# Kernel tuning notes

Hardware: AMD Instinct MI355X
Metric: run time of the kernel (lower is better)

## Reference

```python
import jax, jax.numpy as jnp
import numpy as np

B, T, D = 64, 196, 768
H = 12          # num_heads
HID = 64        # lstm hidden dim per direction


def setup_inputs() -> dict:
    key = jax.random.key(0)
    ks = jax.random.split(key, 13)
    s = 0.02
    return {
        "x": jax.random.normal(ks[0], (B, T, D), jnp.float32),
        "pre_W": jax.random.normal(ks[1], (D, D), jnp.float32) * s,
        "pre_b": jax.random.normal(ks[2], (D,), jnp.float32) * s,
        "Wih_f": jax.random.normal(ks[3], (H, 4 * HID, D // H), jnp.float32) * s,
        "Whh_f": jax.random.normal(ks[4], (H, 4 * HID, HID), jnp.float32) * s,
        "bih_f": jax.random.normal(ks[5], (H, 4 * HID), jnp.float32) * s,
        "bhh_f": jax.random.normal(ks[6], (H, 4 * HID), jnp.float32) * s,
        "Wih_r": jax.random.normal(ks[7], (H, 4 * HID, D // H), jnp.float32) * s,
        "Whh_r": jax.random.normal(ks[8], (H, 4 * HID, HID), jnp.float32) * s,
        "bih_r": jax.random.normal(ks[9], (H, 4 * HID), jnp.float32) * s,
        "bhh_r": jax.random.normal(ks[10], (H, 4 * HID), jnp.float32) * s,
        "proj_W": jax.random.normal(ks[11], (D, 2 * H * HID), jnp.float32) * s,
        "proj_b": jax.random.normal(ks[12], (D,), jnp.float32) * s,
    }


def _lstm_dir(xh, Wih, Whh, bih, bhh):
    """xh: [H, B, T, d]; weights stacked over heads. Returns [H, B, T, HID].
    Gate order i, f, g, o (PyTorch convention)."""
    hid = Whh.shape[-1]

    def one_head(xc, wih, whh, bi, bh):
        # precompute input contribution for all timesteps: [B, T, 4*hid]
        gx = jnp.einsum('btd,gd->btg', xc, wih) + bi + bh

        def step(carry, g_t):
            h, c = carry
            g = g_t + h @ whh.T
            i, f, gg, o = jnp.split(g, 4, axis=-1)
            i = jax.nn.sigmoid(i)
            f = jax.nn.sigmoid(f)
            gg = jnp.tanh(gg)
            o = jax.nn.sigmoid(o)
            c = f * c + i * gg
            h = o * jnp.tanh(c)
            return (h, c), h

        b = xc.shape[0]
        h0 = jnp.zeros((b, hid), xc.dtype)
        _, hs = jax.lax.scan(step, (h0, h0), gx.transpose(1, 0, 2))  # [T, B, hid]
        return hs.transpose(1, 0, 2)  # [B, T, hid]

    return jax.vmap(one_head)(xh, Wih, Whh, bih, bhh)


def reference(x, pre_W, pre_b, Wih_f, Whh_f, bih_f, bhh_f,
              Wih_r, Whh_r, bih_r, bhh_r, proj_W, proj_b):
    x = x @ pre_W.T + pre_b                      # pre_proj
    b, t, dm = x.shape
    h = Wih_f.shape[0]
    d = dm // h
    xh = x.reshape(b, t, h, d).transpose(2, 0, 1, 3)   # [H, B, T, d] (chunk along last dim)

    y_f = _lstm_dir(xh, Wih_f, Whh_f, bih_f, bhh_f)               # [H, B, T, hid]
    y_r = _lstm_dir(xh[:, :, ::-1], Wih_r, Whh_r, bih_r, bhh_r)[:, :, ::-1]

    hid = y_f.shape[-1]
    # concat fwd outputs of all heads, then rev outputs of all heads
    yf = y_f.transpose(1, 2, 0, 3).reshape(b, t, h * hid)
    yr = y_r.transpose(1, 2, 0, 3).reshape(b, t, h * hid)
    y_cat = jnp.concatenate([yf, yr], axis=-1)   # [B, T, 2*H*hid]
    return y_cat @ proj_W.T + proj_b
```

## Files before the change

kernel.cpp:

```cpp
#include <hip/hip_runtime.h>
#include <hip/hip_bf16.h>
#include <cstdint>
#include <cstddef>

#define B_   64
#define T_   196
#define D_   768
#define H_   12
#define HID_ 64
#define NT_  (B_ * T_)

typedef __attribute__((ext_vector_type(8))) __bf16 bf16x8;
typedef __attribute__((ext_vector_type(4))) float  f32x4;

__device__ __forceinline__ float bf2f(uint16_t u) {
    uint32_t x = ((uint32_t)u) << 16;
    return __builtin_bit_cast(float, x);
}
__device__ __forceinline__ uint16_t f2bf(float f) {
    uint32_t x = __builtin_bit_cast(uint32_t, f);
    uint32_t r = (x + 0x7fffu + ((x >> 16) & 1u)) >> 16;
    return (uint16_t)r;
}
__device__ __forceinline__ __bf16 f2bfv(float f) {
    return __builtin_bit_cast(__bf16, f2bf(f));
}

__device__ __forceinline__ float sigm(float x) {
    return __builtin_amdgcn_rcpf(1.f + __expf(-x));
}
__device__ __forceinline__ float tanh_f(float x) {
    return 1.f - 2.f * __builtin_amdgcn_rcpf(1.f + __expf(2.f * x));
}

__device__ __forceinline__ int swzg(int row, int col) {
    int b = (row << 6) + (col << 1);
    b ^= (row & 7) << 4;
    return b >> 1;
}
__device__ __forceinline__ int swzA(int row, int col) {
    int b = (row << 8) + (col << 1);
    b ^= (row & 7) << 4;
    return b >> 1;
}

__global__ __launch_bounds__(256)
void f32_to_bf16_k(const float* __restrict__ in, uint16_t* __restrict__ out, int n4)
{
    int i = blockIdx.x * 256 + threadIdx.x;
    const int stride = gridDim.x * 256;
    for (; i < n4; i += stride) {
        float4 v = ((const float4*)in)[i];
        ushort4 o;
        o.x = f2bf(v.x); o.y = f2bf(v.y); o.z = f2bf(v.z); o.w = f2bf(v.w);
        ((ushort4*)out)[i] = o;
    }
}

template<int KDIM, bool A_F32, bool OUT_BF16>
__global__ __launch_bounds__(256) __attribute__((amdgpu_waves_per_eu(2)))
void gemm_nt_mfma(const void* __restrict__ Aab, const uint16_t* __restrict__ Bw,
                  const float* __restrict__ bias, void* __restrict__ Cout, int Mtot)
{
    constexpr int NK = KDIM / 32;
    __shared__ uint16_t smA[2][128 * 32];
    __shared__ uint16_t smB[2][128 * 32];

    const int tid = threadIdx.x, lane = tid & 63, wv = tid >> 6;
    const int n0 = blockIdx.x * 128, m0 = blockIdx.y * 128;
    const int wr = wv >> 1, wc = wv & 1;
    const int fr = lane & 15;
    const int fk8 = (lane >> 4) * 8;

    const int srow = tid >> 1;
    const int scol = (tid & 1) * 16;

    const float*    Af = (const float*)Aab;
    const uint16_t* Ab = (const uint16_t*)Aab;

    f32x4 acc[4][4];
#pragma unroll
    for (int i = 0; i < 4; ++i)
#pragma unroll
        for (int j = 0; j < 4; ++j) acc[i][j] = (f32x4){0.f, 0.f, 0.f, 0.f};

    uint4 rA0, rA1, rB0, rB1;

    auto loadA = [&](int k0) {
        if constexpr (A_F32) {
            const float* p = Af + (size_t)(n0 + srow) * KDIM + k0 + scol;
            float4 a0 = *(const float4*)(p);
            float4 a1 = *(const float4*)(p + 4);
            float4 a2 = *(const float4*)(p + 8);
            float4 a3 = *(const float4*)(p + 12);
            rA0.x = (uint32_t)f2bf(a0.x) | ((uint32_t)f2bf(a0.y) << 16);
            rA0.y = (uint32_t)f2bf(a0.z) | ((uint32_t)f2bf(a0.w) << 16);
            rA0.z = (uint32_t)f2bf(a1.x) | ((uint32_t)f2bf(a1.y) << 16);
            rA0.w = (uint32_t)f2bf(a1.z) | ((uint32_t)f2bf(a1.w) << 16);
            rA1.x = (uint32_t)f2bf(a2.x) | ((uint32_t)f2bf(a2.y) << 16);
            rA1.y = (uint32_t)f2bf(a2.z) | ((uint32_t)f2bf(a2.w) << 16);
            rA1.z = (uint32_t)f2bf(a3.x) | ((uint32_t)f2bf(a3.y) << 16);
            rA1.w = (uint32_t)f2bf(a3.z) | ((uint32_t)f2bf(a3.w) << 16);
        } else {
            const uint16_t* p = Ab + (size_t)(n0 + srow) * KDIM + k0 + scol;
            rA0 = *(const uint4*)p;
            rA1 = *(const uint4*)(p + 8);
        }
    };
    auto loadB = [&](int k0) {
        const uint16_t* p = Bw + (size_t)(m0 + srow) * KDIM + k0 + scol;
        rB0 = *(const uint4*)p;
        rB1 = *(const uint4*)(p + 8);
    };
    auto dsWrite = [&](int buf) {
        *(uint4*)&smA[buf][swzg(srow, scol)]     = rA0;
        *(uint4*)&smA[buf][swzg(srow, scol + 8)] = rA1;
        *(uint4*)&smB[buf][swzg(srow, scol)]     = rB0;
        *(uint4*)&smB[buf][swzg(srow, scol + 8)] = rB1;
    };

    loadA(0); loadB(0);
    dsWrite(0);

    for (int kt = 0; kt < NK; ++kt) {
        __syncthreads();
        const int buf = kt & 1;
        const bool more = (kt + 1) < NK;
        if (more) { loadA(32 * (kt + 1)); loadB(32 * (kt + 1)); }

        bf16x8 af[4], bfg[4];
#pragma unroll
        for (int i = 0; i < 4; ++i)
            af[i] = *(const bf16x8*)&smA[buf][swzg(64 * wr + 16 * i + fr, fk8)];
#pragma unroll
        for (int j = 0; j < 4; ++j)
            bfg[j] = *(const bf16x8*)&smB[buf][swzg(64 * wc + 16 * j + fr, fk8)];
#pragma unroll
        for (int i = 0; i < 4; ++i)
#pragma unroll
            for (int j = 0; j < 4; ++j)
                acc[i][j] = __builtin_amdgcn_mfma_f32_16x16x32_bf16(af[i], bfg[j], acc[i][j], 0, 0, 0);

        if (more) dsWrite(buf ^ 1);
    }

    float biasj[4];
#pragma unroll
    for (int j = 0; j < 4; ++j) biasj[j] = bias[m0 + 64 * wc + 16 * j + fr];

#pragma unroll
    for (int i = 0; i < 4; ++i) {
#pragma unroll
        for (int r = 0; r < 4; ++r) {
            const int n = n0 + 64 * wr + 16 * i + (lane >> 4) * 4 + r;
#pragma unroll
            for (int j = 0; j < 4; ++j) {
                const int m = m0 + 64 * wc + 16 * j + fr;
                const float v = acc[i][j][r] + biasj[j];
                if constexpr (OUT_BF16)
                    ((uint16_t*)Cout)[(size_t)n * Mtot + m] = f2bf(v);
                else
                    ((float*)Cout)[(size_t)n * Mtot + m] = v;
            }
        }
    }
}

__global__ __launch_bounds__(256) __attribute__((amdgpu_waves_per_eu(1)))
void lstm_rec_mfma(const uint16_t* __restrict__ xp,
                   const float* __restrict__ Wih_f, const float* __restrict__ Whh_f,
                   const float* __restrict__ bih_f, const float* __restrict__ bhh_f,
                   const float* __restrict__ Wih_r, const float* __restrict__ Whh_r,
                   const float* __restrict__ bih_r, const float* __restrict__ bhh_r,
                   uint16_t* __restrict__ y)
{
    const int blk   = blockIdx.x;
    const int b0    = (blk & 3) * 16;
    const int chain = blk >> 2;
    const int head  = chain % H_;
    const int dir   = chain / H_;
    const int tid   = threadIdx.x;
    const int lane  = tid & 63;
    const int q     = tid >> 6;

    const float* WihP = (dir ? Wih_r : Wih_f) + (size_t)head * 256 * 64;
    const float* WhhP = (dir ? Whh_r : Whh_f) + (size_t)head * 256 * 64;
    const float* bihP = (dir ? bih_r : bih_f) + head * 256;
    const float* bhhP = (dir ? bhh_r : bhh_f) + head * 256;

    __shared__ uint16_t Act[2][16 * 128];

    const int fr = lane & 15;
    const int fk = (lane >> 4) << 3;

    bf16x8 wfrag[4][4];
#pragma unroll
    for (int gi = 0; gi < 4; ++gi) {
        const int row = 16 * q + 64 * gi + fr;
#pragma unroll
        for (int kk = 0; kk < 4; ++kk) {
            const int k0 = 32 * kk + fk;
            const float* src = (k0 < 64) ? (WihP + row * 64 + k0)
                                         : (WhhP + row * 64 + (k0 - 64));
            float4 aa = *(const float4*)(src);
            float4 bb = *(const float4*)(src + 4);
            bf16x8 w;
            w[0] = f2bfv(aa.x); w[1] = f2bfv(aa.y); w[2] = f2bfv(aa.z); w[3] = f2bfv(aa.w);
            w[4] = f2bfv(bb.x); w[5] = f2bfv(bb.y); w[6] = f2bfv(bb.z); w[7] = f2bfv(bb.w);
            wfrag[gi][kk] = w;
        }
    }
#pragma unroll
    for (int gi = 0; gi < 4; ++gi)
#pragma unroll
        for (int kk = 0; kk < 4; ++kk)
            asm volatile("" : "+v"(wfrag[gi][kk]));

    f32x4 binit[4];
#pragma unroll
    for (int gi = 0; gi < 4; ++gi) {
#pragma unroll
        for (int r = 0; r < 4; ++r) {
            const int row = 16 * q + 64 * gi + (lane >> 4) * 4 + r;
            binit[gi][r] = bihP[row] + bhhP[row];
        }
    }

    const int tstep = dir ? -1 : 1;
    const int t0    = dir ? (T_ - 1) : 0;

    const int batch = tid >> 4;
    const int d0    = (tid & 15) * 4;
    {
        uint2 z; z.x = 0; z.y = 0;
        *(uint2*)&Act[0][swzA(batch, 64 + d0)] = z;
        uint2 xv = *(const uint2*)(xp + ((size_t)(b0 + batch) * T_ + t0) * D_ + head * 64 + d0);
        *(uint2*)&Act[0][swzA(batch, d0)] = xv;
    }
    __syncthreads();

    const uint16_t* xptr = xp + ((size_t)(b0 + batch) * T_ + t0) * D_ + head * 64 + d0;
    uint16_t* yptr = y + ((size_t)(b0 + fr) * T_ + t0) * 1536 + dir * 768 + head * 64
                       + 16 * q + ((lane >> 4) << 2);
    const ptrdiff_t xstride = (ptrdiff_t)tstep * D_;
    const ptrdiff_t ystride = (ptrdiff_t)tstep * 1536;

    float cst[4] = {0.f, 0.f, 0.f, 0.f};

    for (int s = 0; s < T_; ++s) {
        uint2 xstage; xstage.x = 0; xstage.y = 0;
        if (s + 1 < T_) { xptr += xstride; xstage = *(const uint2*)xptr; }

        const uint16_t* A0 = Act[s & 1];
        uint16_t*       A1 = Act[(s + 1) & 1];

        f32x4 acc[4];
#pragma unroll
        for (int gi = 0; gi < 4; ++gi) acc[gi] = binit[gi];
#pragma unroll
        for (int kk = 0; kk < 4; ++kk) {
            bf16x8 afr = *(const bf16x8*)&A0[swzA(fr, 32 * kk + fk)];
#pragma unroll
            for (int gi = 0; gi < 4; ++gi)
                acc[gi] = __builtin_amdgcn_mfma_f32_16x16x32_bf16(wfrag[gi][kk], afr, acc[gi], 0, 0, 0);
        }

        ushort4 hpack;
#pragma unroll
        for (int r = 0; r < 4; ++r) {
            const float i_ = sigm(acc[0][r]);
            const float f_ = sigm(acc[1][r]);
            const float g_ = tanh_f(acc[2][r]);
            const float o_ = sigm(acc[3][r]);
            const float c  = f_ * cst[r] + i_ * g_;
            cst[r] = c;
            const float h = o_ * tanh_f(c);
            ((unsigned short*)&hpack)[r] = f2bf(h);
        }

        *(ushort4*)&A1[swzA(fr, 64 + 16 * q + ((lane >> 4) << 2))] = hpack;
        if (s + 1 < T_) *(uint2*)&A1[swzA(batch, d0)] = xstage;

        *(ushort4*)yptr = hpack;
        yptr += ystride;

        __syncthreads();
    }
}

extern "C" void kernel_launch(void* const* d_in, const int* in_sizes, int n_in,
                              void* d_out, int out_size, void* d_ws, size_t ws_size,
                              hipStream_t stream) {
    const float* x      = (const float*)d_in[0];
    const float* pre_W  = (const float*)d_in[1];
    const float* pre_b  = (const float*)d_in[2];
    const float* Wih_f  = (const float*)d_in[3];
    const float* Whh_f  = (const float*)d_in[4];
    const float* bih_f  = (const float*)d_in[5];
    const float* bhh_f  = (const float*)d_in[6];
    const float* Wih_r  = (const float*)d_in[7];
    const float* Whh_r  = (const float*)d_in[8];
    const float* bih_r  = (const float*)d_in[9];
    const float* bhh_r  = (const float*)d_in[10];
    const float* proj_W = (const float*)d_in[11];
    const float* proj_b = (const float*)d_in[12];
    float* out = (float*)d_out;

    uint16_t* xp      = (uint16_t*)d_ws;
    uint16_t* y       = xp + (size_t)NT_ * D_;
    uint16_t* preWbf  = y + (size_t)NT_ * 1536;
    uint16_t* projWbf = preWbf + (size_t)D_ * D_;

    f32_to_bf16_k<<<256, 256, 0, stream>>>(pre_W, preWbf, D_ * D_ / 4);
    f32_to_bf16_k<<<256, 256, 0, stream>>>(proj_W, projWbf, D_ * 1536 / 4);

    dim3 g1(NT_ / 128, D_ / 128);
    gemm_nt_mfma<768, true, true><<<g1, 256, 0, stream>>>(x, preWbf, pre_b, xp, D_);

    lstm_rec_mfma<<<96, 256, 0, stream>>>(xp, Wih_f, Whh_f, bih_f, bhh_f,
                                          Wih_r, Whh_r, bih_r, bhh_r, y);

    dim3 g3(NT_ / 128, D_ / 128);
    gemm_nt_mfma<1536, false, false><<<g3, 256, 0, stream>>>(y, projWbf, proj_b, out, D_);
}
```

Before: 329.3 us.

## Use direct global-to-LDS loads in GEMMs and pre-convert x to bf16

```diff
diff --git a/kernel.cpp b/kernel.cpp
--- a/kernel.cpp
+++ b/kernel.cpp
@@ -13,6 +13,9 @@
 typedef __attribute__((ext_vector_type(8))) __bf16 bf16x8;
 typedef __attribute__((ext_vector_type(4))) float  f32x4;
 
+typedef __attribute__((address_space(1))) const void* gas_t;
+typedef __attribute__((address_space(3))) void*       las_t;
+
 __device__ __forceinline__ float bf2f(uint16_t u) {
     uint32_t x = ((uint32_t)u) << 16;
     return __builtin_bit_cast(float, x);
@@ -33,11 +36,6 @@
     return 1.f - 2.f * __builtin_amdgcn_rcpf(1.f + __expf(2.f * x));
 }
 
-__device__ __forceinline__ int swzg(int row, int col) {
-    int b = (row << 6) + (col << 1);
-    b ^= (row & 7) << 4;
-    return b >> 1;
-}
 __device__ __forceinline__ int swzA(int row, int col) {
     int b = (row << 8) + (col << 1);
     b ^= (row & 7) << 4;
@@ -57,10 +55,10 @@
     }
 }
 
-template<int KDIM, bool A_F32, bool OUT_BF16>
-__global__ __launch_bounds__(256) __attribute__((amdgpu_waves_per_eu(2)))
-void gemm_nt_mfma(const void* __restrict__ Aab, const uint16_t* __restrict__ Bw,
-                  const float* __restrict__ bias, void* __restrict__ Cout, int Mtot)
+template<int KDIM, bool OUT_BF16>
+__global__ __launch_bounds__(256)
+void gemm_nt_gl(const uint16_t* __restrict__ A, const uint16_t* __restrict__ Bw,
+                const float* __restrict__ bias, void* __restrict__ Cout, int Mtot)
 {
     constexpr int NK = KDIM / 32;
     __shared__ uint16_t smA[2][128 * 32];
@@ -72,11 +70,19 @@
     const int fr = lane & 15;
     const int fk8 = (lane >> 4) * 8;
 
-    const int srow = tid >> 1;
-    const int scol = (tid & 1) * 16;
-
-    const float*    Af = (const float*)Aab;
-    const uint16_t* Ab = (const uint16_t*)Aab;
+    const int sr = lane >> 2;
+    const int sc = (lane & 3) * 8;
+
+    auto stage = [&](int buf, int k0) {
+#pragma unroll
+        for (int i = 0; i < 2; ++i) {
+            const int r0 = 16 * wv + 64 * i;
+            const uint16_t* ga = A  + (size_t)(n0 + r0 + sr) * KDIM + k0 + sc;
+            const uint16_t* gb = Bw + (size_t)(m0 + r0 + sr) * KDIM + k0 + sc;
+            __builtin_amdgcn_global_load_lds((gas_t)ga, (las_t)&smA[buf][r0 * 32], 16, 0, 0);
+            __builtin_amdgcn_global_load_lds((gas_t)gb, (las_t)&smB[buf][r0 * 32], 16, 0, 0);
+        }
+    };
 
     f32x4 acc[4][4];
 #pragma unroll
@@ -84,64 +90,25 @@
 #pragma unroll
         for (int j = 0; j < 4; ++j) acc[i][j] = (f32x4){0.f, 0.f, 0.f, 0.f};
 
-    uint4 rA0, rA1, rB0, rB1;
-
-    auto loadA = [&](int k0) {
-        if constexpr (A_F32) {
-            const float* p = Af + (size_t)(n0 + srow) * KDIM + k0 + scol;
-            float4 a0 = *(const float4*)(p);
-            float4 a1 = *(const float4*)(p + 4);
-            float4 a2 = *(const float4*)(p + 8);
-            float4 a3 = *(const float4*)(p + 12);
-            rA0.x = (uint32_t)f2bf(a0.x) | ((uint32_t)f2bf(a0.y) << 16);
-            rA0.y = (uint32_t)f2bf(a0.z) | ((uint32_t)f2bf(a0.w) << 16);
-            rA0.z = (uint32_t)f2bf(a1.x) | ((uint32_t)f2bf(a1.y) << 16);
-            rA0.w = (uint32_t)f2bf(a1.z) | ((uint32_t)f2bf(a1.w) << 16);
-            rA1.x = (uint32_t)f2bf(a2.x) | ((uint32_t)f2bf(a2.y) << 16);
-            rA1.y = (uint32_t)f2bf(a2.z) | ((uint32_t)f2bf(a2.w) << 16);
-            rA1.z = (uint32_t)f2bf(a3.x) | ((uint32_t)f2bf(a3.y) << 16);
-            rA1.w = (uint32_t)f2bf(a3.z) | ((uint32_t)f2bf(a3.w) << 16);
-        } else {
-            const uint16_t* p = Ab + (size_t)(n0 + srow) * KDIM + k0 + scol;
-            rA0 = *(const uint4*)p;
-            rA1 = *(const uint4*)(p + 8);
-        }
-    };
-    auto loadB = [&](int k0) {
-        const uint16_t* p = Bw + (size_t)(m0 + srow) * KDIM + k0 + scol;
-        rB0 = *(const uint4*)p;
-        rB1 = *(const uint4*)(p + 8);
-    };
-    auto dsWrite = [&](int buf) {
-        *(uint4*)&smA[buf][swzg(srow, scol)]     = rA0;
-        *(uint4*)&smA[buf][swzg(srow, scol + 8)] = rA1;
-        *(uint4*)&smB[buf][swzg(srow, scol)]     = rB0;
-        *(uint4*)&smB[buf][swzg(srow, scol + 8)] = rB1;
-    };
-
-    loadA(0); loadB(0);
-    dsWrite(0);
+    stage(0, 0);
 
     for (int kt = 0; kt < NK; ++kt) {
+        const int buf = kt & 1;
         __syncthreads();
-        const int buf = kt & 1;
-        const bool more = (kt + 1) < NK;
-        if (more) { loadA(32 * (kt + 1)); loadB(32 * (kt + 1)); }
+        if (kt + 1 < NK) stage(buf ^ 1, 32 * (kt + 1));
 
         bf16x8 af[4], bfg[4];
 #pragma unroll
         for (int i = 0; i < 4; ++i)
-            af[i] = *(const bf16x8*)&smA[buf][swzg(64 * wr + 16 * i + fr, fk8)];
+            af[i] = *(const bf16x8*)&smA[buf][(64 * wr + 16 * i + fr) * 32 + fk8];
 #pragma unroll
         for (int j = 0; j < 4; ++j)
-            bfg[j] = *(const bf16x8*)&smB[buf][swzg(64 * wc + 16 * j + fr, fk8)];
+            bfg[j] = *(const bf16x8*)&smB[buf][(64 * wc + 16 * j + fr) * 32 + fk8];
 #pragma unroll
         for (int i = 0; i < 4; ++i)
 #pragma unroll
             for (int j = 0; j < 4; ++j)
                 acc[i][j] = __builtin_amdgcn_mfma_f32_16x16x32_bf16(af[i], bfg[j], acc[i][j], 0, 0, 0);
-
-        if (more) dsWrite(buf ^ 1);
     }
 
     float biasj[4];
@@ -246,8 +213,12 @@
     const ptrdiff_t ystride = (ptrdiff_t)tstep * 1536;
 
     float cst[4] = {0.f, 0.f, 0.f, 0.f};
+    ushort4 hprev;
+    uint16_t* yprev = nullptr;
 
     for (int s = 0; s < T_; ++s) {
+        if (s > 0) *(ushort4*)yprev = hprev;
+
         uint2 xstage; xstage.x = 0; xstage.y = 0;
         if (s + 1 < T_) { xptr += xstride; xstage = *(const uint2*)xptr; }
 
@@ -281,11 +252,13 @@
         *(ushort4*)&A1[swzA(fr, 64 + 16 * q + ((lane >> 4) << 2))] = hpack;
         if (s + 1 < T_) *(uint2*)&A1[swzA(batch, d0)] = xstage;
 
-        *(ushort4*)yptr = hpack;
+        hprev = hpack;
+        yprev = yptr;
         yptr += ystride;
 
         __syncthreads();
     }
+    *(ushort4*)yprev = hprev;
 }
 
 extern "C" void kernel_launch(void* const* d_in, const int* in_sizes, int n_in,
@@ -310,16 +283,18 @@
     uint16_t* y       = xp + (size_t)NT_ * D_;
     uint16_t* preWbf  = y + (size_t)NT_ * 1536;
     uint16_t* projWbf = preWbf + (size_t)D_ * D_;
+    uint16_t* xbf     = y;
 
     f32_to_bf16_k<<<256, 256, 0, stream>>>(pre_W, preWbf, D_ * D_ / 4);
     f32_to_bf16_k<<<256, 256, 0, stream>>>(proj_W, projWbf, D_ * 1536 / 4);
+    f32_to_bf16_k<<<2048, 256, 0, stream>>>(x, xbf, NT_ * D_ / 4);
 
     dim3 g1(NT_ / 128, D_ / 128);
-    gemm_nt_mfma<768, true, true><<<g1, 256, 0, stream>>>(x, preWbf, pre_b, xp, D_);
+    gemm_nt_gl<768, true><<<g1, 256, 0, stream>>>(xbf, preWbf, pre_b, xp, D_);
 
     lstm_rec_mfma<<<96, 256, 0, stream>>>(xp, Wih_f, Whh_f, bih_f, bhh_f,
                                           Wih_r, Whh_r, bih_r, bhh_r, y);
 
     dim3 g3(NT_ / 128, D_ / 128);
-    gemm_nt_mfma<1536, false, false><<<g3, 256, 0, stream>>>(y, projWbf, proj_b, out, D_);
-}
+    gemm_nt_gl<1536, false><<<g3, 256, 0, stream>>>(y, projWbf, proj_b, out, D_);
+}
```

Result: faster. 312.9 us (-5.0%).
